# Performance work log

Hardware: AMD Instinct MI355X
Metric: run time of the kernel (lower is better)

## Reference

```python
import math
import jax, jax.numpy as jnp
import numpy as np

B, T, D = 2, 2048, 2048
NH, HD = 16, 48           # query heads, head dim
LAT, NLH = 256, 8         # latent dim, latent (kv) heads
EPS = 1e-5


def setup_inputs() -> dict:
    key = jax.random.key(0)
    ks = jax.random.split(key, 7)
    x = jax.random.normal(ks[0], (B, T, D), dtype=jnp.float32)
    # causal mask [B, 1, T, T]
    mask = jnp.broadcast_to(jnp.tril(jnp.ones((T, T), dtype=bool))[None, None], (B, 1, T, T))
    s = lambda fan_in: 1.0 / math.sqrt(fan_in)
    Wq = jax.random.normal(ks[1], (D, NH * HD), dtype=jnp.float32) * s(D)
    Wkv = jax.random.normal(ks[2], (D, LAT), dtype=jnp.float32) * s(D)
    w_norm = jnp.ones((LAT,), dtype=jnp.float32)
    Wk = jax.random.normal(ks[3], (LAT, NLH * HD), dtype=jnp.float32) * s(LAT)
    Wv = jax.random.normal(ks[4], (LAT, NLH * HD), dtype=jnp.float32) * s(LAT)
    Wo = jax.random.normal(ks[5], (NH * HD, D), dtype=jnp.float32) * s(NH * HD)
    return {"x": x, "mask": mask, "Wq": Wq, "Wkv": Wkv, "w_norm": w_norm,
            "Wk": Wk, "Wv": Wv, "Wo": Wo}


def rms_norm(x, weight, eps=EPS):
    var = jnp.mean(x * x, axis=-1, keepdims=True)
    return x * jax.lax.rsqrt(var + eps) * weight


def reference(x, mask, Wq, Wkv, w_norm, Wk, Wv, Wo):
    b, t, _ = x.shape
    q = (x @ Wq).reshape(b, t, NH, HD)                      # [B,T,NH,HD]
    kv_latent = rms_norm(x @ Wkv, w_norm)                   # [B,T,LAT]
    k = (kv_latent @ Wk).reshape(b, t, NLH, HD)             # [B,T,NLH,HD]
    v = (kv_latent @ Wv).reshape(b, t, NLH, HD)
    rep = NH // NLH
    k = jnp.repeat(k, rep, axis=2)                          # [B,T,NH,HD]
    v = jnp.repeat(v, rep, axis=2)
    q = q.transpose(0, 2, 1, 3)                             # [B,NH,T,HD]
    k = k.transpose(0, 2, 1, 3)
    v = v.transpose(0, 2, 1, 3)
    scale = 1.0 / math.sqrt(HD)
    scores = jnp.einsum('bhqd,bhkd->bhqk', q, k) * scale    # [B,NH,T,T]
    scores = jnp.where(mask, scores, -1e9)
    attn = jax.nn.softmax(scores, axis=-1)
    out = jnp.einsum('bhqk,bhkd->bhqd', attn, v)            # [B,NH,T,HD]
    out = out.transpose(0, 2, 1, 3).reshape(b, t, NH * HD)
    return out @ Wo                                          # [B,T,D]
```

## Files before the change

### kernel.cpp

```cpp
#include <hip/hip_runtime.h>
#include <hip/hip_bf16.h>

typedef __hip_bfloat16 bf16;
typedef __attribute__((ext_vector_type(8))) short short8;
typedef __attribute__((ext_vector_type(4))) float f32x4;

#define Bq   2
#define Tq   2048
#define Dq   2048
#define NHq  16
#define HDq  48
#define LATq 256
#define NLHq 8
#define QN   (NHq * HDq)
#define KVN  (NLHq * HDq)

__device__ __forceinline__ unsigned short f2u(float x) {
    __hip_bfloat16 h = __float2bfloat16(x);
    return *reinterpret_cast<unsigned short*>(&h);
}
__device__ __forceinline__ float u2f(unsigned short u) {
    return __uint_as_float((unsigned)u << 16);
}
__device__ __forceinline__ unsigned pk2(float a, float b) {
    return (unsigned)f2u(a) | ((unsigned)f2u(b) << 16);
}
__device__ __forceinline__ void cstore(bf16* C, size_t i, float v) { C[i] = __float2bfloat16(v); }
__device__ __forceinline__ void cstore(float* C, size_t i, float v) { C[i] = v; }

__global__ void __launch_bounds__(256)
cvt_x(const float* __restrict__ in, bf16* __restrict__ out) {
    const size_t i = ((size_t)blockIdx.x * 256 + threadIdx.x) * 8;
    const float4 a = *(const float4*)&in[i];
    const float4 b = *(const float4*)&in[i + 4];
    uint4 u;
    u.x = pk2(a.x, a.y); u.y = pk2(a.z, a.w);
    u.z = pk2(b.x, b.y); u.w = pk2(b.z, b.w);
    *(uint4*)&out[i] = u;
}

__global__ void __launch_bounds__(256)
tr_w(const float* __restrict__ W, bf16* __restrict__ WT, int K, int N) {
    __shared__ float ts[32][33];
    const int n0 = blockIdx.x * 32, k0 = blockIdx.y * 32;
    const int t = threadIdx.x;
    const int r = t >> 3, c4 = (t & 7) * 4;
    const float4 v = *(const float4*)&W[(size_t)(k0 + r) * N + n0 + c4];
    ts[r][c4] = v.x; ts[r][c4 + 1] = v.y; ts[r][c4 + 2] = v.z; ts[r][c4 + 3] = v.w;
    __syncthreads();
    const unsigned u0 = pk2(ts[c4][r], ts[c4 + 1][r]);
    const unsigned u1 = pk2(ts[c4 + 2][r], ts[c4 + 3][r]);
    *(uint2*)&WT[(size_t)(n0 + r) * K + k0 + c4] = make_uint2(u0, u1);
}

template<typename CT>
__global__ void __launch_bounds__(256)
gemm_bt128(const bf16* __restrict__ A, const bf16* __restrict__ BT,
           CT* __restrict__ C, int K, int NC) {
    __shared__ short As[128 * 40];
    __shared__ short Bs[64 * 40];
    const int t  = threadIdx.x;
    const int m0 = blockIdx.x * 128;
    const int n0 = blockIdx.y * 64;
    const int w  = t >> 6;
    const int wm = (w & 1) * 64;
    const int wn = (w >> 1) * 32;
    const int lr = t & 15;
    const int quad = (t >> 4) & 3;
    const int am = t >> 2, ac = t & 3;

    f32x4 acc[4][2];
    #pragma unroll
    for (int mi = 0; mi < 4; ++mi)
        #pragma unroll
        for (int ni = 0; ni < 2; ++ni) acc[mi][ni] = (f32x4){0.f, 0.f, 0.f, 0.f};

    int aoff[4], boff[2];
    #pragma unroll
    for (int mi = 0; mi < 4; ++mi) aoff[mi] = (wm + mi * 16 + lr) * 40 + quad * 8;
    #pragma unroll
    for (int ni = 0; ni < 2; ++ni) boff[ni] = (wn + ni * 16 + lr) * 40 + quad * 8;

    for (int kt = 0; kt < K / 32; ++kt) {
        const int kb = kt * 32 + ac * 8;
        *(uint4*)&As[am * 40 + ac * 8] = *(const uint4*)&A[(size_t)(m0 + am) * K + kb];
        *(uint4*)&As[(am + 64) * 40 + ac * 8] = *(const uint4*)&A[(size_t)(m0 + am + 64) * K + kb];
        *(uint4*)&Bs[am * 40 + ac * 8] = *(const uint4*)&BT[(size_t)(n0 + am) * K + kb];
        __syncthreads();
        short8 af[4], bfr[2];
        #pragma unroll
        for (int mi = 0; mi < 4; ++mi) af[mi] = *(const short8*)&As[aoff[mi]];
        #pragma unroll
        for (int ni = 0; ni < 2; ++ni) bfr[ni] = *(const short8*)&Bs[boff[ni]];
        #pragma unroll
        for (int mi = 0; mi < 4; ++mi)
            #pragma unroll
            for (int ni = 0; ni < 2; ++ni)
                acc[mi][ni] = __builtin_amdgcn_mfma_f32_16x16x32_bf16(af[mi], bfr[ni], acc[mi][ni], 0, 0, 0);
        __syncthreads();
    }
    #pragma unroll
    for (int mi = 0; mi < 4; ++mi)
        #pragma unroll
        for (int ni = 0; ni < 2; ++ni) {
            const int col = n0 + wn + ni * 16 + lr;
            #pragma unroll
            for (int r = 0; r < 4; ++r) {
                const int row = m0 + wm + mi * 16 + quad * 4 + r;
                cstore(C, (size_t)row * NC + col, acc[mi][ni][r]);
            }
        }
}

template<typename CT>
__global__ void __launch_bounds__(256)
gemm_bt64(const bf16* __restrict__ A, const bf16* __restrict__ BT,
          CT* __restrict__ C, int K, int NC) {
    __shared__ short As[64 * 40];
    __shared__ short Bs[64 * 40];
    const int t  = threadIdx.x;
    const int m0 = blockIdx.x * 64;
    const int n0 = blockIdx.y * 64;
    const int w  = t >> 6;
    const int wm = (w & 1) * 32;
    const int wn = (w >> 1) * 32;
    const int lr = t & 15;
    const int quad = (t >> 4) & 3;
    const int am = t >> 2, ac = t & 3;

    f32x4 acc[2][2];
    #pragma unroll
    for (int mi = 0; mi < 2; ++mi)
        #pragma unroll
        for (int ni = 0; ni < 2; ++ni) acc[mi][ni] = (f32x4){0.f, 0.f, 0.f, 0.f};

    int aoff[2], boff[2];
    #pragma unroll
    for (int mi = 0; mi < 2; ++mi) aoff[mi] = (wm + mi * 16 + lr) * 40 + quad * 8;
    #pragma unroll
    for (int ni = 0; ni < 2; ++ni) boff[ni] = (wn + ni * 16 + lr) * 40 + quad * 8;

    for (int kt = 0; kt < K / 32; ++kt) {
        const int kb = kt * 32 + ac * 8;
        *(uint4*)&As[am * 40 + ac * 8] = *(const uint4*)&A[(size_t)(m0 + am) * K + kb];
        *(uint4*)&Bs[am * 40 + ac * 8] = *(const uint4*)&BT[(size_t)(n0 + am) * K + kb];
        __syncthreads();
        short8 af[2], bfr[2];
        #pragma unroll
        for (int mi = 0; mi < 2; ++mi) af[mi] = *(const short8*)&As[aoff[mi]];
        #pragma unroll
        for (int ni = 0; ni < 2; ++ni) bfr[ni] = *(const short8*)&Bs[boff[ni]];
        #pragma unroll
        for (int mi = 0; mi < 2; ++mi)
            #pragma unroll
            for (int ni = 0; ni < 2; ++ni)
                acc[mi][ni] = __builtin_amdgcn_mfma_f32_16x16x32_bf16(af[mi], bfr[ni], acc[mi][ni], 0, 0, 0);
        __syncthreads();
    }
    #pragma unroll
    for (int mi = 0; mi < 2; ++mi)
        #pragma unroll
        for (int ni = 0; ni < 2; ++ni) {
            const int col = n0 + wn + ni * 16 + lr;
            #pragma unroll
            for (int r = 0; r < 4; ++r) {
                const int row = m0 + wm + mi * 16 + quad * 4 + r;
                cstore(C, (size_t)row * NC + col, acc[mi][ni][r]);
            }
        }
}

__global__ void __launch_bounds__(256)
mla_kvrms(const float* __restrict__ xkv, const float* __restrict__ wn,
          bf16* __restrict__ lat) {
    const int t = threadIdx.x;
    const int row = blockIdx.x * 4 + (t >> 6);
    const int lane = t & 63;
    const float4 v = *(const float4*)&xkv[(size_t)row * LATq + lane * 4];
    float ss = v.x * v.x + v.y * v.y + v.z * v.z + v.w * v.w;
    ss += __shfl_xor(ss, 1);  ss += __shfl_xor(ss, 2);  ss += __shfl_xor(ss, 4);
    ss += __shfl_xor(ss, 8);  ss += __shfl_xor(ss, 16); ss += __shfl_xor(ss, 32);
    const float rr = rsqrtf(ss * (1.0f / LATq) + 1e-5f);
    const float4 g = *(const float4*)&wn[lane * 4];
    const unsigned w0 = pk2(v.x * rr * g.x, v.y * rr * g.y);
    const unsigned w1 = pk2(v.z * rr * g.z, v.w * rr * g.w);
    *(uint2*)&lat[(size_t)row * LATq + lane * 4] = make_uint2(w0, w1);
}

__global__ void __launch_bounds__(256)
mla_attn(const bf16* __restrict__ q, const bf16* __restrict__ kk,
         const bf16* __restrict__ vv, bf16* __restrict__ ao) {
    __shared__ __align__(16) short Ks[2][64 * 48];
    __shared__ __align__(16) short Vt[2][48 * 72];
    __shared__ __align__(16) short Ps[4][2 * 16 * 72];
    const int t    = threadIdx.x;
    const int g    = blockIdx.x;
    const int qy   = blockIdx.y;
    const int b    = blockIdx.z;
    const int qt0  = (qy < 16) ? (qy << 1) : (63 - (qy << 1));
    const int qt   = b ? (31 - qt0) : qt0;
    const int w    = t >> 6;
    const int lane = t & 63;
    const int lr   = t & 15;
    const int quad = (t >> 4) & 3;
    const int hh   = w & 1;
    const int rh   = w >> 1;
    const int h    = g * 2 + hh;
    const int Q0   = qt * 64;
    const float scale = 0.14433756729740643f;
    const short8 z8 = {0, 0, 0, 0, 0, 0, 0, 0};

    short8 qf[2][2];
    int qg[2];
    #pragma unroll
    for (int st = 0; st < 2; ++st) {
        qg[st] = Q0 + rh * 32 + st * 16 + lr;
        const bf16* qr = q + (size_t)(b * Tq + qg[st]) * QN + h * HDq;
        qf[st][0] = *(const short8*)(qr + quad * 8);
        const short8 q1 = *(const short8*)(qr + 32 + (quad & 1) * 8);
        qf[st][1] = (quad < 2) ? q1 : z8;
    }

    const bf16* kb = kk + (size_t)b * Tq * KVN + g * HDq;
    const bf16* vb = vv + (size_t)b * Tq * KVN + g * HDq;

    float m[2] = {-1e30f, -1e30f}, l[2] = {0.f, 0.f};
    f32x4 acc[2][3];
    #pragma unroll
    for (int st = 0; st < 2; ++st)
        #pragma unroll
        for (int dm = 0; dm < 3; ++dm) acc[st][dm] = (f32x4){0.f, 0.f, 0.f, 0.f};

    short* Pw = &Ps[w][0];
    uint4 pre[3];

    auto issue = [&](int tl) {
        #pragma unroll
        for (int r = 0; r < 3; ++r) {
            if (w < 2) {
                const int idx = (w * 3 + r) * 64 + lane;
                const int row = idx / 6, ch = idx - row * 6;
                pre[r] = *(const uint4*)(kb + (size_t)(tl * 64 + row) * KVN + ch * 8);
            } else {
                const int idx = ((w - 2) * 3 + r) * 64 + lane;
                const int kp = idx & 31, hc = idx >> 5;
                const bf16* src = vb + (size_t)(tl * 64 + 2 * kp) * KVN + hc * 4;
                const uint2 a2 = *(const uint2*)src;
                const uint2 b2 = *(const uint2*)(src + KVN);
                pre[r].x = a2.x; pre[r].y = a2.y; pre[r].z = b2.x; pre[r].w = b2.y;
            }
        }
    };
    auto lwrite = [&](int bb) {
        #pragma unroll
        for (int r = 0; r < 3; ++r) {
            if (w < 2) {
                const int idx = (w * 3 + r) * 64 + lane;
                const int row = idx / 6, ch = idx - row * 6;
                *(uint4*)&Ks[bb][row * 48 + ch * 8] = pre[r];
            } else {
                const int idx = ((w - 2) * 3 + r) * 64 + lane;
                const int kp = idx & 31, hc = idx >> 5;
                const unsigned short* u = (const unsigned short*)&pre[r];
                #pragma unroll
                for (int j = 0; j < 4; ++j)
                    *(unsigned*)&Vt[bb][(hc * 4 + j) * 72 + 2 * kp] =
                        (unsigned)u[j] | ((unsigned)u[4 + j] << 16);
            }
        }
    };

    issue(0);
    lwrite(0);
    __syncthreads();
    int cur = 0;

    for (int tl = 0; tl <= qt; ++tl) {
        const bool pref = (tl < qt);
        if (pref) issue(tl + 1);

        f32x4 sc[2][4];
        #pragma unroll
        for (int mt = 0; mt < 4; ++mt) {
            const short8 k0 = *(const short8*)&Ks[cur][(mt * 16 + lr) * 48 + quad * 8];
            const short8 k1v = *(const short8*)&Ks[cur][(mt * 16 + lr) * 48 + 32 + (quad & 1) * 8];
            const short8 k1 = (quad < 2) ? k1v : z8;
            #pragma unroll
            for (int st = 0; st < 2; ++st) {
                f32x4 s = (f32x4){0.f, 0.f, 0.f, 0.f};
                s = __builtin_amdgcn_mfma_f32_16x16x32_bf16(k0, qf[st][0], s, 0, 0, 0);
                s = __builtin_amdgcn_mfma_f32_16x16x32_bf16(k1, qf[st][1], s, 0, 0, 0);
                sc[st][mt] = s;
            }
        }
        if (tl == qt) {
            #pragma unroll
            for (int st = 0; st < 2; ++st) {
                const int qloc = rh * 32 + st * 16 + lr;
                #pragma unroll
                for (int mt = 0; mt < 4; ++mt)
                    #pragma unroll
                    for (int r = 0; r < 4; ++r)
                        if (mt * 16 + quad * 4 + r > qloc) sc[st][mt][r] = -1e30f;
            }
        }
        #pragma unroll
        for (int st = 0; st < 2; ++st) {
            float mx = -1e30f;
            #pragma unroll
            for (int mt = 0; mt < 4; ++mt)
                #pragma unroll
                for (int r = 0; r < 4; ++r) mx = fmaxf(mx, sc[st][mt][r]);
            mx = fmaxf(mx, __shfl_xor(mx, 16));
            mx = fmaxf(mx, __shfl_xor(mx, 32));
            const float mn = fmaxf(m[st], mx * scale);
            const float f  = __expf(m[st] - mn);
            m[st] = mn;
            float rs = 0.f;
            #pragma unroll
            for (int mt = 0; mt < 4; ++mt)
                #pragma unroll
                for (int r = 0; r < 4; ++r) {
                    const float p = u2f(f2u(__expf(fmaf(sc[st][mt][r], scale, -mn))));
                    sc[st][mt][r] = p;
                    rs += p;
                }
            rs += __shfl_xor(rs, 16);
            rs += __shfl_xor(rs, 32);
            l[st] = l[st] * f + rs;
            #pragma unroll
            for (int dm = 0; dm < 3; ++dm)
                #pragma unroll
                for (int r = 0; r < 4; ++r) acc[st][dm][r] *= f;
            short* Pst = Pw + st * 16 * 72;
            #pragma unroll
            for (int mt = 0; mt < 4; ++mt) {
                unsigned* pw = (unsigned*)&Pst[lr * 72 + mt * 16 + quad * 4];
                pw[0] = pk2(sc[st][mt][0], sc[st][mt][1]);
                pw[1] = pk2(sc[st][mt][2], sc[st][mt][3]);
            }
        }
        short8 pf[2][2];
        #pragma unroll
        for (int st = 0; st < 2; ++st) {
            const short* Pst = Pw + st * 16 * 72;
            pf[st][0] = *(const short8*)&Pst[lr * 72 + quad * 8];
            pf[st][1] = *(const short8*)&Pst[lr * 72 + 32 + quad * 8];
        }
        #pragma unroll
        for (int dm = 0; dm < 3; ++dm) {
            const short8 v0 = *(const short8*)&Vt[cur][(dm * 16 + lr) * 72 + quad * 8];
            const short8 v1 = *(const short8*)&Vt[cur][(dm * 16 + lr) * 72 + 32 + quad * 8];
            #pragma unroll
            for (int st = 0; st < 2; ++st) {
                acc[st][dm] = __builtin_amdgcn_mfma_f32_16x16x32_bf16(v0, pf[st][0], acc[st][dm], 0, 0, 0);
                acc[st][dm] = __builtin_amdgcn_mfma_f32_16x16x32_bf16(v1, pf[st][1], acc[st][dm], 0, 0, 0);
            }
        }

        if (pref) lwrite(cur ^ 1);
        __syncthreads();
        cur ^= 1;
    }

    #pragma unroll
    for (int st = 0; st < 2; ++st) {
        const float inv = 1.0f / l[st];
        bf16* orow = ao + (size_t)(b * Tq + qg[st]) * QN + h * HDq;
        #pragma unroll
        for (int dm = 0; dm < 3; ++dm) {
            const unsigned w0 = pk2(acc[st][dm][0] * inv, acc[st][dm][1] * inv);
            const unsigned w1 = pk2(acc[st][dm][2] * inv, acc[st][dm][3] * inv);
            *(uint2*)(orow + dm * 16 + quad * 4) = make_uint2(w0, w1);
        }
    }
}

extern "C" void kernel_launch(void* const* d_in, const int* in_sizes, int n_in,
                              void* d_out, int out_size, void* d_ws, size_t ws_size,
                              hipStream_t stream) {
    const float* x   = (const float*)d_in[0];
    const float* Wq  = (const float*)d_in[2];
    const float* Wkv = (const float*)d_in[3];
    const float* wn  = (const float*)d_in[4];
    const float* Wk  = (const float*)d_in[5];
    const float* Wv  = (const float*)d_in[6];
    const float* Wo  = (const float*)d_in[7];
    float* out = (float*)d_out;

    const int M = Bq * Tq;
    char* ob = (char*)d_out;
    bf16*  xb   = (bf16*)ob;
    bf16*  qws  = (bf16*)(ob + 16777216);
    float* xkv  = (float*)(ob + 23068672);
    bf16*  latb = (bf16*)(ob + 27262976);
    bf16*  WqT  = (bf16*)(ob + 29360128);
    bf16*  WkvT = (bf16*)(ob + 32505856);
    bf16*  WkT  = (bf16*)ob;
    bf16*  WvT  = (bf16*)(ob + 393216);
    bf16*  kws = (bf16*)d_ws;
    bf16*  vws = kws + (size_t)M * KVN;
    bf16*  aob = vws + (size_t)M * KVN;
    bf16*  WoT = (bf16*)d_ws;

    cvt_x <<<4096, 256, 0, stream>>>(x, xb);
    tr_w  <<<dim3(QN / 32, Dq / 32), 256, 0, stream>>>(Wq, WqT, Dq, QN);
    tr_w  <<<dim3(LATq / 32, Dq / 32), 256, 0, stream>>>(Wkv, WkvT, Dq, LATq);
    gemm_bt128<bf16> <<<dim3(M / 128, QN / 64), 256, 0, stream>>>(xb, WqT, qws, Dq, QN);
    gemm_bt64<float> <<<dim3(M / 64, LATq / 64), 256, 0, stream>>>(xb, WkvT, xkv, Dq, LATq);
    tr_w  <<<dim3(KVN / 32, LATq / 32), 256, 0, stream>>>(Wk, WkT, LATq, KVN);
    tr_w  <<<dim3(KVN / 32, LATq / 32), 256, 0, stream>>>(Wv, WvT, LATq, KVN);
    mla_kvrms <<<M / 4, 256, 0, stream>>>(xkv, wn, latb);
    gemm_bt64<bf16> <<<dim3(M / 64, KVN / 64), 256, 0, stream>>>(latb, WkT, kws, LATq, KVN);
    gemm_bt64<bf16> <<<dim3(M / 64, KVN / 64), 256, 0, stream>>>(latb, WvT, vws, LATq, KVN);
    mla_attn <<<dim3(NLHq, 32, Bq), 256, 0, stream>>>(qws, kws, vws, aob);
    tr_w  <<<dim3(Dq / 32, QN / 32), 256, 0, stream>>>(Wo, WoT, QN, Dq);
    gemm_bt128<float> <<<dim3(M / 128, Dq / 64), 256, 0, stream>>>(aob, WoT, out, QN, Dq);
}
```

Before: 320.9 us.

## Fuse Q/KV-latent and K/V projection GEMMs into unified 128x128 prefetching GEMM

Concatenates transposed Wq and Wkv (and Wk and Wv) so each pair of projections runs as one GEMM launch, with the epilogue routing columns to separate outputs. The GEMM tile grows from 128x64 to 128x128, and the next K-slice is loaded into registers while the current one is computed. This is meant to cut launch count and give more data reuse per tile. In exchange it raises register use and lowers the number of blocks, which can hurt occupancy on the smaller GEMMs.

```diff
diff --git a/kernel.cpp b/kernel.cpp
--- a/kernel.cpp
+++ b/kernel.cpp
@@ -25,8 +25,6 @@
 __device__ __forceinline__ unsigned pk2(float a, float b) {
     return (unsigned)f2u(a) | ((unsigned)f2u(b) << 16);
 }
-__device__ __forceinline__ void cstore(bf16* C, size_t i, float v) { C[i] = __float2bfloat16(v); }
-__device__ __forceinline__ void cstore(float* C, size_t i, float v) { C[i] = v; }
 
 __global__ void __launch_bounds__(256)
 cvt_x(const float* __restrict__ in, bf16* __restrict__ out) {
@@ -53,119 +51,87 @@
     *(uint2*)&WT[(size_t)(n0 + r) * K + k0 + c4] = make_uint2(u0, u1);
 }
 
-template<typename CT>
-__global__ void __launch_bounds__(256)
-gemm_bt128(const bf16* __restrict__ A, const bf16* __restrict__ BT,
-           CT* __restrict__ C, int K, int NC) {
+template<int MODE>
+__global__ void __launch_bounds__(256)
+gemm128(const bf16* __restrict__ A, const bf16* __restrict__ BT,
+        void* __restrict__ C0v, void* __restrict__ C1v, int K) {
     __shared__ short As[128 * 40];
-    __shared__ short Bs[64 * 40];
+    __shared__ short Bs[128 * 40];
     const int t  = threadIdx.x;
     const int m0 = blockIdx.x * 128;
-    const int n0 = blockIdx.y * 64;
+    const int n0 = blockIdx.y * 128;
     const int w  = t >> 6;
     const int wm = (w & 1) * 64;
-    const int wn = (w >> 1) * 32;
+    const int wn = (w >> 1) * 64;
     const int lr = t & 15;
     const int quad = (t >> 4) & 3;
-    const int am = t >> 2, ac = t & 3;
-
-    f32x4 acc[4][2];
+
+    f32x4 acc[4][4];
     #pragma unroll
     for (int mi = 0; mi < 4; ++mi)
         #pragma unroll
-        for (int ni = 0; ni < 2; ++ni) acc[mi][ni] = (f32x4){0.f, 0.f, 0.f, 0.f};
-
-    int aoff[4], boff[2];
+        for (int ni = 0; ni < 4; ++ni) acc[mi][ni] = (f32x4){0.f, 0.f, 0.f, 0.f};
+
+    int aoff[4], boff[4];
     #pragma unroll
     for (int mi = 0; mi < 4; ++mi) aoff[mi] = (wm + mi * 16 + lr) * 40 + quad * 8;
     #pragma unroll
-    for (int ni = 0; ni < 2; ++ni) boff[ni] = (wn + ni * 16 + lr) * 40 + quad * 8;
-
-    for (int kt = 0; kt < K / 32; ++kt) {
-        const int kb = kt * 32 + ac * 8;
-        *(uint4*)&As[am * 40 + ac * 8] = *(const uint4*)&A[(size_t)(m0 + am) * K + kb];
-        *(uint4*)&As[(am + 64) * 40 + ac * 8] = *(const uint4*)&A[(size_t)(m0 + am + 64) * K + kb];
-        *(uint4*)&Bs[am * 40 + ac * 8] = *(const uint4*)&BT[(size_t)(n0 + am) * K + kb];
+    for (int ni = 0; ni < 4; ++ni) boff[ni] = (wn + ni * 16 + lr) * 40 + quad * 8;
+
+    uint4 pa[2], pb[2];
+    auto glo = [&](int kt) {
+        #pragma unroll
+        for (int it = 0; it < 2; ++it) {
+            const int idx = t + 256 * it;
+            const int row = idx >> 2, ch = idx & 3;
+            pa[it] = *(const uint4*)&A[(size_t)(m0 + row) * K + kt * 32 + ch * 8];
+            pb[it] = *(const uint4*)&BT[(size_t)(n0 + row) * K + kt * 32 + ch * 8];
+        }
+    };
+
+    const int nk = K / 32;
+    glo(0);
+    for (int kt = 0; kt < nk; ++kt) {
+        #pragma unroll
+        for (int it = 0; it < 2; ++it) {
+            const int idx = t + 256 * it;
+            const int row = idx >> 2, ch = idx & 3;
+            *(uint4*)&As[row * 40 + ch * 8] = pa[it];
+            *(uint4*)&Bs[row * 40 + ch * 8] = pb[it];
+        }
         __syncthreads();
-        short8 af[4], bfr[2];
+        if (kt + 1 < nk) glo(kt + 1);
+        short8 af[4], bfr[4];
         #pragma unroll
         for (int mi = 0; mi < 4; ++mi) af[mi] = *(const short8*)&As[aoff[mi]];
         #pragma unroll
-        for (int ni = 0; ni < 2; ++ni) bfr[ni] = *(const short8*)&Bs[boff[ni]];
+        for (int ni = 0; ni < 4; ++ni) bfr[ni] = *(const short8*)&Bs[boff[ni]];
         #pragma unroll
         for (int mi = 0; mi < 4; ++mi)
             #pragma unroll
-            for (int ni = 0; ni < 2; ++ni)
+            for (int ni = 0; ni < 4; ++ni)
                 acc[mi][ni] = __builtin_amdgcn_mfma_f32_16x16x32_bf16(af[mi], bfr[ni], acc[mi][ni], 0, 0, 0);
         __syncthreads();
     }
+
     #pragma unroll
     for (int mi = 0; mi < 4; ++mi)
         #pragma unroll
-        for (int ni = 0; ni < 2; ++ni) {
+        for (int ni = 0; ni < 4; ++ni) {
             const int col = n0 + wn + ni * 16 + lr;
             #pragma unroll
             for (int r = 0; r < 4; ++r) {
                 const int row = m0 + wm + mi * 16 + quad * 4 + r;
-                cstore(C, (size_t)row * NC + col, acc[mi][ni][r]);
-            }
-        }
-}
-
-template<typename CT>
-__global__ void __launch_bounds__(256)
-gemm_bt64(const bf16* __restrict__ A, const bf16* __restrict__ BT,
-          CT* __restrict__ C, int K, int NC) {
-    __shared__ short As[64 * 40];
-    __shared__ short Bs[64 * 40];
-    const int t  = threadIdx.x;
-    const int m0 = blockIdx.x * 64;
-    const int n0 = blockIdx.y * 64;
-    const int w  = t >> 6;
-    const int wm = (w & 1) * 32;
-    const int wn = (w >> 1) * 32;
-    const int lr = t & 15;
-    const int quad = (t >> 4) & 3;
-    const int am = t >> 2, ac = t & 3;
-
-    f32x4 acc[2][2];
-    #pragma unroll
-    for (int mi = 0; mi < 2; ++mi)
-        #pragma unroll
-        for (int ni = 0; ni < 2; ++ni) acc[mi][ni] = (f32x4){0.f, 0.f, 0.f, 0.f};
-
-    int aoff[2], boff[2];
-    #pragma unroll
-    for (int mi = 0; mi < 2; ++mi) aoff[mi] = (wm + mi * 16 + lr) * 40 + quad * 8;
-    #pragma unroll
-    for (int ni = 0; ni < 2; ++ni) boff[ni] = (wn + ni * 16 + lr) * 40 + quad * 8;
-
-    for (int kt = 0; kt < K / 32; ++kt) {
-        const int kb = kt * 32 + ac * 8;
-        *(uint4*)&As[am * 40 + ac * 8] = *(const uint4*)&A[(size_t)(m0 + am) * K + kb];
-        *(uint4*)&Bs[am * 40 + ac * 8] = *(const uint4*)&BT[(size_t)(n0 + am) * K + kb];
-        __syncthreads();
-        short8 af[2], bfr[2];
-        #pragma unroll
-        for (int mi = 0; mi < 2; ++mi) af[mi] = *(const short8*)&As[aoff[mi]];
-        #pragma unroll
-        for (int ni = 0; ni < 2; ++ni) bfr[ni] = *(const short8*)&Bs[boff[ni]];
-        #pragma unroll
-        for (int mi = 0; mi < 2; ++mi)
-            #pragma unroll
-            for (int ni = 0; ni < 2; ++ni)
-                acc[mi][ni] = __builtin_amdgcn_mfma_f32_16x16x32_bf16(af[mi], bfr[ni], acc[mi][ni], 0, 0, 0);
-        __syncthreads();
-    }
-    #pragma unroll
-    for (int mi = 0; mi < 2; ++mi)
-        #pragma unroll
-        for (int ni = 0; ni < 2; ++ni) {
-            const int col = n0 + wn + ni * 16 + lr;
-            #pragma unroll
-            for (int r = 0; r < 4; ++r) {
-                const int row = m0 + wm + mi * 16 + quad * 4 + r;
-                cstore(C, (size_t)row * NC + col, acc[mi][ni][r]);
+                const float v = acc[mi][ni][r];
+                if constexpr (MODE == 0) {
+                    if (col < QN) ((bf16*)C0v)[(size_t)row * QN + col] = __float2bfloat16(v);
+                    else ((float*)C1v)[(size_t)row * LATq + (col - QN)] = v;
+                } else if constexpr (MODE == 1) {
+                    if (col < KVN) ((bf16*)C0v)[(size_t)row * KVN + col] = __float2bfloat16(v);
+                    else ((bf16*)C1v)[(size_t)row * KVN + (col - KVN)] = __float2bfloat16(v);
+                } else {
+                    ((float*)C0v)[(size_t)row * Dq + col] = v;
+                }
             }
         }
 }
@@ -390,30 +356,26 @@
 
     const int M = Bq * Tq;
     char* ob = (char*)d_out;
-    bf16*  xb   = (bf16*)ob;
-    bf16*  qws  = (bf16*)(ob + 16777216);
-    float* xkv  = (float*)(ob + 23068672);
-    bf16*  latb = (bf16*)(ob + 27262976);
-    bf16*  WqT  = (bf16*)(ob + 29360128);
-    bf16*  WkvT = (bf16*)(ob + 32505856);
-    bf16*  WkT  = (bf16*)ob;
-    bf16*  WvT  = (bf16*)(ob + 393216);
+    bf16*  xb    = (bf16*)ob;
+    bf16*  qws   = (bf16*)(ob + 16777216);
+    float* xkv   = (float*)(ob + 23068672);
+    bf16*  latb  = (bf16*)(ob + 27262976);
+    bf16*  WqkvT = (bf16*)(ob + 29360128);
+    bf16*  WkvpT = (bf16*)ob;
     bf16*  kws = (bf16*)d_ws;
     bf16*  vws = kws + (size_t)M * KVN;
     bf16*  aob = vws + (size_t)M * KVN;
     bf16*  WoT = (bf16*)d_ws;
 
     cvt_x <<<4096, 256, 0, stream>>>(x, xb);
-    tr_w  <<<dim3(QN / 32, Dq / 32), 256, 0, stream>>>(Wq, WqT, Dq, QN);
-    tr_w  <<<dim3(LATq / 32, Dq / 32), 256, 0, stream>>>(Wkv, WkvT, Dq, LATq);
-    gemm_bt128<bf16> <<<dim3(M / 128, QN / 64), 256, 0, stream>>>(xb, WqT, qws, Dq, QN);
-    gemm_bt64<float> <<<dim3(M / 64, LATq / 64), 256, 0, stream>>>(xb, WkvT, xkv, Dq, LATq);
-    tr_w  <<<dim3(KVN / 32, LATq / 32), 256, 0, stream>>>(Wk, WkT, LATq, KVN);
-    tr_w  <<<dim3(KVN / 32, LATq / 32), 256, 0, stream>>>(Wv, WvT, LATq, KVN);
+    tr_w  <<<dim3(QN / 32, Dq / 32), 256, 0, stream>>>(Wq, WqkvT, Dq, QN);
+    tr_w  <<<dim3(LATq / 32, Dq / 32), 256, 0, stream>>>(Wkv, WqkvT + (size_t)QN * Dq, Dq, LATq);
+    gemm128<0> <<<dim3(M / 128, 1024 / 128), 256, 0, stream>>>(xb, WqkvT, qws, xkv, Dq);
+    tr_w  <<<dim3(KVN / 32, LATq / 32), 256, 0, stream>>>(Wk, WkvpT, LATq, KVN);
+    tr_w  <<<dim3(KVN / 32, LATq / 32), 256, 0, stream>>>(Wv, WkvpT + (size_t)KVN * LATq, LATq, KVN);
     mla_kvrms <<<M / 4, 256, 0, stream>>>(xkv, wn, latb);
-    gemm_bt64<bf16> <<<dim3(M / 64, KVN / 64), 256, 0, stream>>>(latb, WkT, kws, LATq, KVN);
-    gemm_bt64<bf16> <<<dim3(M / 64, KVN / 64), 256, 0, stream>>>(latb, WvT, vws, LATq, KVN);
+    gemm128<1> <<<dim3(M / 128, 768 / 128), 256, 0, stream>>>(latb, WkvpT, kws, vws, LATq);
     mla_attn <<<dim3(NLHq, 32, Bq), 256, 0, stream>>>(qws, kws, vws, aob);
     tr_w  <<<dim3(Dq / 32, QN / 32), 256, 0, stream>>>(Wo, WoT, QN, Dq);
-    gemm_bt128<float> <<<dim3(M / 128, Dq / 64), 256, 0, stream>>>(aob, WoT, out, QN, Dq);
-}
+    gemm128<2> <<<dim3(M / 128, Dq / 128), 256, 0, stream>>>(aob, WoT, out, nullptr, QN);
+}
```

Result: slower. 377.9 us (+17.8%).
